# Kernel optimization log

Measured on AMD Instinct MI355X. Metric: run time of the kernel, lower is better.

## Reference

```python
import jax, jax.numpy as jnp
import numpy as np

NUM_HEADS = 4
HEAD_DIM = 64  # out_dim // num_heads
NEG_INF = -9e15


def setup_inputs() -> dict:
    key = jax.random.key(0)
    k1, k2, k3, k4 = jax.random.split(key, 4)
    b, n, in_dim, out_dim = 8, 1024, 256, 256
    x = jax.random.normal(k1, (b, n, in_dim), dtype=jnp.float32)
    adj = jax.random.uniform(k2, (b, n, n), dtype=jnp.float32)
    # linear_proj weight, stored as [in_dim, out_dim] (xavier-ish scale)
    Wp = jax.random.normal(k3, (in_dim, out_dim), dtype=jnp.float32) * (1.0 / np.sqrt(in_dim))
    # scoring_fn weight for concat([left(64), right(64), adj(1)]) -> 1
    Ws = jax.random.normal(k4, (2 * HEAD_DIM + 1,), dtype=jnp.float32) * (1.0 / np.sqrt(HEAD_DIM))
    bias = jnp.zeros((out_dim,), dtype=jnp.float32)
    return {"x": x, "adj": adj, "Wp": Wp, "Ws": Ws, "bias": bias}


def reference(x, adj, Wp, Ws, bias):
    b, n, _ = x.shape
    H, hd = NUM_HEADS, HEAD_DIM
    # manifold_in = Euclidean -> logmap0 is identity; dropout is eval (p=0)
    proj = (x @ Wp).reshape(b, n, H, hd)  # [b,n,H,hd]
    # scoring_fn(cat[left, right, adj]) decomposed: score = left.w_l + right.w_r + adj*w_a
    w_l, w_r, w_a = Ws[:hd], Ws[hd:2 * hd], Ws[2 * hd]
    s_l = jnp.einsum('bnhd,d->bnh', proj, w_l)  # dest-node term
    s_r = jnp.einsum('bmhd,d->bmh', proj, w_r)  # src-node term
    score = s_l[:, :, None, :] + s_r[:, None, :, :] + (adj * w_a)[..., None]  # [b,n,n,H]
    score = jax.nn.leaky_relu(score, 0.2)
    # local_agg: mask out non-edges (adj <= 1e-5) by adding -9e15
    pad = (adj <= 1e-5).astype(score.dtype)
    score = score + (NEG_INF * pad)[..., None]
    att = jax.nn.softmax(score, axis=2)  # softmax over source nodes m
    # msg[b,i,h,d] = sum_m att[b,i,m,h] * proj[b,m,h,d]
    msg = jnp.einsum('bimh,bmhd->bihd', att, proj).reshape(b, n, H * hd)
    # in_dim == out_dim -> no skip_proj; Euclidean expmap0/transp0/expmap: out = x + msg + bias
    out = x + msg + bias
    out = jax.nn.leaky_relu(out, 0.5)  # act = LeakyReLU(0.5)
    return out, adj
```

## Files before the change

kernel.cpp:

```cpp
#include <hip/hip_runtime.h>

#define NHEADS 4
#define HDIM   64
#define BATCH  8
#define SEQ    1024
#define CH     256
#define LOG2E  1.4426950408889634f
#define MC     128
#define LDP    132

typedef float  f32x4  __attribute__((ext_vector_type(4)));
typedef __bf16 bf16x8 __attribute__((ext_vector_type(8)));
typedef short  s16x8  __attribute__((ext_vector_type(8)));
union FU { s16x8 s; bf16x8 b; };

__device__ inline unsigned short f2bf(float f) {
    unsigned u = __float_as_uint(f);
    return (unsigned short)((u + 0x7fffu + ((u >> 16) & 1u)) >> 16);
}
__device__ inline float4 nt_load4(const float* p) {
    f32x4 v = __builtin_nontemporal_load(reinterpret_cast<const f32x4*>(p));
    return make_float4(v.x, v.y, v.z, v.w);
}
__device__ inline void nt_store4(float* p, float4 v) {
    f32x4 u = {v.x, v.y, v.z, v.w};
    __builtin_nontemporal_store(u, reinterpret_cast<f32x4*>(p));
}


__global__ __launch_bounds__(256) void wpt_cast(const float* __restrict__ Wp,
                                                unsigned short* __restrict__ WpT) {
    __shared__ float T[32][33];
    const int t = threadIdx.x;
    const int kt = blockIdx.x * 32, ct = blockIdx.y * 32;
    const int r = t >> 3, c4 = (t & 7) * 4;
    float4 v = *reinterpret_cast<const float4*>(&Wp[(size_t)(kt + r) * CH + ct + c4]);
    T[r][c4 + 0] = v.x; T[r][c4 + 1] = v.y; T[r][c4 + 2] = v.z; T[r][c4 + 3] = v.w;
    __syncthreads();
    unsigned p0 = (unsigned)f2bf(T[c4 + 0][r]) | ((unsigned)f2bf(T[c4 + 1][r]) << 16);
    unsigned p1 = (unsigned)f2bf(T[c4 + 2][r]) | ((unsigned)f2bf(T[c4 + 3][r]) << 16);
    uint2 o = make_uint2(p0, p1);
    *reinterpret_cast<uint2*>(&WpT[(size_t)(ct + r) * CH + kt + c4]) = o;
}

__global__ __launch_bounds__(256, 2) void proj_fused(const float* __restrict__ x,
                                                     const unsigned short* __restrict__ WpT,
                                                     const float* __restrict__ Ws,
                                                     unsigned short* __restrict__ projT,
                                                     float* __restrict__ sl,
                                                     float* __restrict__ sr) {
    const int t = threadIdx.x, w = t >> 6, l = t & 63, il = l & 15, g = l >> 4;
    const int row0 = blockIdx.x * 16;
    const int b = row0 >> 10, n0 = row0 & 1023;

    const unsigned short* Ap = WpT + (size_t)(w * 64 + il) * CH + g * 8;
    const float*          Bp = x + (size_t)(row0 + il) * CH + g * 8;

    float4 xv[8][2];
#pragma unroll
    for (int kt = 0; kt < 8; ++kt) {
        xv[kt][0] = *reinterpret_cast<const float4*>(Bp + kt * 32);
        xv[kt][1] = *reinterpret_cast<const float4*>(Bp + kt * 32 + 4);
    }

    f32x4 acc[4] = {};
#pragma unroll
    for (int kt = 0; kt < 8; ++kt) {
        FU a[4], bb;
#pragma unroll
        for (int ai = 0; ai < 4; ++ai)
            a[ai].s = *reinterpret_cast<const s16x8*>(Ap + (size_t)ai * 16 * CH + kt * 32);
        bb.b[0] = (__bf16)xv[kt][0].x; bb.b[1] = (__bf16)xv[kt][0].y;
        bb.b[2] = (__bf16)xv[kt][0].z; bb.b[3] = (__bf16)xv[kt][0].w;
        bb.b[4] = (__bf16)xv[kt][1].x; bb.b[5] = (__bf16)xv[kt][1].y;
        bb.b[6] = (__bf16)xv[kt][1].z; bb.b[7] = (__bf16)xv[kt][1].w;
#pragma unroll
        for (int ai = 0; ai < 4; ++ai)
            acc[ai] = __builtin_amdgcn_mfma_f32_16x16x32_bf16(a[ai].b, bb.b, acc[ai], 0, 0, 0);
    }

    unsigned short* pS = projT + (((size_t)(b * NHEADS + w)) << 16)
                       + (size_t)(n0 >> 4) * 1024 + (il >> 3) * 128 + (il & 7);
#pragma unroll
    for (int ai = 0; ai < 4; ++ai)
#pragma unroll
        for (int q = 0; q < 4; ++q)
            pS[ai * 256 + (g * 4 + q) * 8] = f2bf(acc[ai][q]);

    float pl = 0.f, pr = 0.f;
#pragma unroll
    for (int ai = 0; ai < 4; ++ai) {
        float4 wlv = *reinterpret_cast<const float4*>(&Ws[ai * 16 + g * 4]);
        float4 wrv = *reinterpret_cast<const float4*>(&Ws[HDIM + ai * 16 + g * 4]);
        pl += acc[ai][0] * wlv.x + acc[ai][1] * wlv.y + acc[ai][2] * wlv.z + acc[ai][3] * wlv.w;
        pr += acc[ai][0] * wrv.x + acc[ai][1] * wrv.y + acc[ai][2] * wrv.z + acc[ai][3] * wrv.w;
    }
    pl += __shfl_xor(pl, 16); pl += __shfl_xor(pl, 32);
    pr += __shfl_xor(pr, 16); pr += __shfl_xor(pr, 32);
    if (l < 16) {
        sl[(size_t)(b * NHEADS + w) * SEQ + n0 + il] = pl * LOG2E;
        sr[(size_t)(b * NHEADS + w) * SEQ + n0 + il] = pr * LOG2E;
    }
}

template <bool FUSE_ADJ>
__global__ __launch_bounds__(512, 2) void attn13(const float* __restrict__ x,
                                                 const float* __restrict__ adj,
                                                 const unsigned short* __restrict__ projT,
                                                 const float* __restrict__ sl,
                                                 const float* __restrict__ sr,
                                                 const float* __restrict__ Ws,
                                                 const float* __restrict__ bias,
                                                 float* __restrict__ out,
                                                 float* __restrict__ out_adj) {
    __shared__ __align__(16) float abuf[2][2][16][LDP];

    const int t = threadIdx.x;
    const int w = t >> 6, l = t & 63, il = l & 15, g = l >> 4;
    const int h = w & 3, mh = w >> 2;
    const int b  = blockIdx.x & 7;
    const int i0 = (blockIdx.x >> 3) * 16;
    const float wa2 = Ws[2 * HDIM] * LOG2E;

    const int sh = t >> 8;
    const int str = (t >> 4) & 15;
    const int stc = (t & 15) * 4;
    const size_t astg = ((size_t)(b * SEQ + i0 + str)) * SEQ + sh * 512 + stc;

    const float sl_i = sl[(size_t)(b * NHEADS + h) * SEQ + i0 + il];
    const float* srp = sr + (size_t)(b * NHEADS + h) * SEQ + mh * 512;
    const unsigned short* pTsw = projT + (((size_t)(b * NHEADS + h)) << 16)
                               + (size_t)mh * 32768
                               + (g >> 1) * 1024 + (g & 1) * 128 + il * 8;

    FU ones;
#pragma unroll
    for (int j = 0; j < 8; ++j) ones.s[j] = (short)0x3F80;

    f32x4 acc[4] = {};
    f32x4 dacc = {};

    float4 c00 = nt_load4(adj + astg);
    float4 c01 = nt_load4(adj + astg + 64);
    float4 cur0 = nt_load4(adj + astg + MC);
    float4 cur1 = nt_load4(adj + astg + MC + 64);
    if (FUSE_ADJ) {
        nt_store4(out_adj + astg, c00);
        nt_store4(out_adj + astg + 64, c01);
    }
    *reinterpret_cast<float4*>(&abuf[0][sh][str][stc])      = c00;
    *reinterpret_cast<float4*>(&abuf[0][sh][str][stc + 64]) = c01;
    __syncthreads();

    for (int c = 0; c < 4; ++c) {
        float4 nx0 = {}, nx1 = {};
        if (c + 2 < 4) {
            nx0 = nt_load4(adj + astg + (size_t)(c + 2) * MC);
            nx1 = nt_load4(adj + astg + (size_t)(c + 2) * MC + 64);
        }
        const float* aT = &abuf[c & 1][mh][il][0];
        const int mt = c * MC;

        float4 av[4][2], sv4[4][2];
        FU B[4][4];
#pragma unroll
        for (int kq = 0; kq < 4; ++kq) {
            const int mk = kq * 32 + g * 8;
            av[kq][0]  = *reinterpret_cast<const float4*>(aT + mk);
            av[kq][1]  = *reinterpret_cast<const float4*>(aT + mk + 4);
            sv4[kq][0] = *reinterpret_cast<const float4*>(srp + mt + mk);
            sv4[kq][1] = *reinterpret_cast<const float4*>(srp + mt + mk + 4);
        }
#pragma unroll
        for (int kq = 0; kq < 4; ++kq) {
#pragma unroll
            for (int bj = 0; bj < 4; ++bj)
                B[kq][bj].s = *reinterpret_cast<const s16x8*>(
                    pTsw + c * 8192 + kq * 2048 + bj * 256);
        }

        FU af[4];
#pragma unroll
        for (int kq = 0; kq < 4; ++kq) {
            float aj[8] = {av[kq][0].x, av[kq][0].y, av[kq][0].z, av[kq][0].w,
                           av[kq][1].x, av[kq][1].y, av[kq][1].z, av[kq][1].w};
            float sv[8] = {sv4[kq][0].x, sv4[kq][0].y, sv4[kq][0].z, sv4[kq][0].w,
                           sv4[kq][1].x, sv4[kq][1].y, sv4[kq][1].z, sv4[kq][1].w};
#pragma unroll
            for (int j = 0; j < 8; ++j) {
                float s = fmaf(aj[j], wa2, sl_i + sv[j]);
                s = __builtin_amdgcn_fmed3f(s, 0.2f * s, 86.5617f);
                float e = (aj[j] <= 1e-5f) ? 0.f : __builtin_amdgcn_exp2f(s);
                af[kq].b[j] = (__bf16)e;
            }
        }

#pragma unroll
        for (int kq = 0; kq < 4; ++kq) {
            acc[0] = __builtin_amdgcn_mfma_f32_16x16x32_bf16(af[kq].b, B[kq][0].b, acc[0], 0, 0, 0);
            acc[1] = __builtin_amdgcn_mfma_f32_16x16x32_bf16(af[kq].b, B[kq][1].b, acc[1], 0, 0, 0);
            acc[2] = __builtin_amdgcn_mfma_f32_16x16x32_bf16(af[kq].b, B[kq][2].b, acc[2], 0, 0, 0);
            acc[3] = __builtin_amdgcn_mfma_f32_16x16x32_bf16(af[kq].b, B[kq][3].b, acc[3], 0, 0, 0);
            dacc   = __builtin_amdgcn_mfma_f32_16x16x32_bf16(af[kq].b, ones.b,   dacc,   0, 0, 0);
        }

        if (c + 1 < 4) {
            if (FUSE_ADJ) {
                nt_store4(out_adj + astg + (size_t)(c + 1) * MC, cur0);
                nt_store4(out_adj + astg + (size_t)(c + 1) * MC + 64, cur1);
            }
            *reinterpret_cast<float4*>(&abuf[(c + 1) & 1][sh][str][stc])      = cur0;
            *reinterpret_cast<float4*>(&abuf[(c + 1) & 1][sh][str][stc + 64]) = cur1;
        }
        __syncthreads();
        cur0 = nx0; cur1 = nx1;
    }

    float (*part)[16][68] = reinterpret_cast<float (*)[16][68]>(&abuf[0][0][0][0]);
    if (mh == 1) {
#pragma unroll
        for (int bj = 0; bj < 4; ++bj)
#pragma unroll
            for (int q = 0; q < 4; ++q)
                part[h][g * 4 + q][bj * 16 + il] = acc[bj][q];
        if (il == 0) {
#pragma unroll
            for (int q = 0; q < 4; ++q) part[h][g * 4 + q][64] = dacc[q];
        }
    }
    __syncthreads();
    if (mh == 0) {
        const float* bb = bias + h * HDIM;
#pragma unroll
        for (int q = 0; q < 4; ++q) {
            const int row = g * 4 + q;
            const float den = dacc[q] + part[h][row][64];
            const float inv = 1.f / den;
            const size_t ob = ((size_t)(b * SEQ + i0 + row)) * CH + h * HDIM + il;
#pragma unroll
            for (int bj = 0; bj < 4; ++bj) {
                float m = acc[bj][q] + part[h][row][bj * 16 + il];
                float v = fmaf(m, inv, x[ob + bj * 16] + bb[bj * 16 + il]);
                v = fmaxf(v, 0.5f * v);
                __builtin_nontemporal_store(v, out + ob + bj * 16);
            }
        }
    }
}

__global__ void adjcopy(const float* __restrict__ adj, float* __restrict__ dst, int n4) {
    int idx = blockIdx.x * blockDim.x + threadIdx.x;
    int stride = gridDim.x * blockDim.x;
    const float4* s = reinterpret_cast<const float4*>(adj);
    float4* d = reinterpret_cast<float4*>(dst);
    for (int i = idx; i < n4; i += stride) d[i] = s[i];
}

extern "C" void kernel_launch(void* const* d_in, const int* in_sizes, int n_in,
                              void* d_out, int out_size, void* d_ws, size_t ws_size,
                              hipStream_t stream) {
    const float* x    = (const float*)d_in[0];
    const float* adj  = (const float*)d_in[1];
    const float* Wp   = (const float*)d_in[2];
    const float* Ws   = (const float*)d_in[3];
    const float* bias = (const float*)d_in[4];
    float* out     = (float*)d_out;
    float* out_adj = out + (size_t)BATCH * SEQ * CH;

    const size_t nProj = (size_t)BATCH * SEQ * CH;
    const size_t nSc   = (size_t)BATCH * NHEADS * SEQ;
    const size_t need  = CH * CH * 2 + nProj * 2 + 2 * nSc * 4;
    const bool use_ws  = (ws_size >= need);
    char* scratch = use_ws ? (char*)d_ws : (char*)out_adj;
    unsigned short* WpT   = (unsigned short*)scratch;
    unsigned short* projT = (unsigned short*)(scratch + (size_t)CH * CH * 2);
    float*          sl    = (float*)(scratch + (size_t)CH * CH * 2 + nProj * 2);
    float*          sr    = sl + nSc;

    wpt_cast<<<dim3(8, 8), 256, 0, stream>>>(Wp, WpT);
    proj_fused<<<dim3(512), 256, 0, stream>>>(x, WpT, Ws, projT, sl, sr);
    if (use_ws) {
        attn13<true><<<dim3(512), 512, 0, stream>>>(
            x, adj, projT, sl, sr, Ws, bias, out, out_adj);
    } else {
        attn13<false><<<dim3(512), 512, 0, stream>>>(
            x, adj, projT, sl, sr, Ws, bias, out, out_adj);
        adjcopy<<<2048, 256, 0, stream>>>(adj, out_adj, (BATCH * SEQ * SEQ) / 4);
    }
}
```

Before: 51.26 us.

## Move adj passthrough copy into projection kernel and use cached adj loads

```diff
diff --git a/kernel.cpp b/kernel.cpp
--- a/kernel.cpp
+++ b/kernel.cpp
@@ -17,10 +17,6 @@
 __device__ inline unsigned short f2bf(float f) {
     unsigned u = __float_as_uint(f);
     return (unsigned short)((u + 0x7fffu + ((u >> 16) & 1u)) >> 16);
-}
-__device__ inline float4 nt_load4(const float* p) {
-    f32x4 v = __builtin_nontemporal_load(reinterpret_cast<const f32x4*>(p));
-    return make_float4(v.x, v.y, v.z, v.w);
 }
 __device__ inline void nt_store4(float* p, float4 v) {
     f32x4 u = {v.x, v.y, v.z, v.w};
@@ -43,12 +39,15 @@
     *reinterpret_cast<uint2*>(&WpT[(size_t)(ct + r) * CH + kt + c4]) = o;
 }
 
+template <bool COPY>
 __global__ __launch_bounds__(256, 2) void proj_fused(const float* __restrict__ x,
                                                      const unsigned short* __restrict__ WpT,
                                                      const float* __restrict__ Ws,
+                                                     const float* __restrict__ adj,
                                                      unsigned short* __restrict__ projT,
                                                      float* __restrict__ sl,
-                                                     float* __restrict__ sr) {
+                                                     float* __restrict__ sr,
+                                                     float* __restrict__ out_adj) {
     const int t = threadIdx.x, w = t >> 6, l = t & 63, il = l & 15, g = l >> 4;
     const int row0 = blockIdx.x * 16;
     const int b = row0 >> 10, n0 = row0 & 1023;
@@ -101,18 +100,31 @@
         sl[(size_t)(b * NHEADS + w) * SEQ + n0 + il] = pl * LOG2E;
         sr[(size_t)(b * NHEADS + w) * SEQ + n0 + il] = pr * LOG2E;
     }
-}
-
-template <bool FUSE_ADJ>
-__global__ __launch_bounds__(512, 2) void attn13(const float* __restrict__ x,
+
+    if (COPY) {
+        const float4* csrc = reinterpret_cast<const float4*>(adj) + (size_t)blockIdx.x * 4096;
+        float*        cdst = out_adj + (size_t)blockIdx.x * 16384;
+#pragma unroll
+        for (int sweep = 0; sweep < 2; ++sweep) {
+            float4 C[8];
+#pragma unroll
+            for (int k = 0; k < 8; ++k)
+                C[k] = csrc[sweep * 2048 + k * 256 + t];
+#pragma unroll
+            for (int k = 0; k < 8; ++k)
+                nt_store4(cdst + (size_t)(sweep * 2048 + k * 256 + t) * 4, C[k]);
+        }
+    }
+}
+
+__global__ __launch_bounds__(512, 2) void attn15(const float* __restrict__ x,
                                                  const float* __restrict__ adj,
                                                  const unsigned short* __restrict__ projT,
                                                  const float* __restrict__ sl,
                                                  const float* __restrict__ sr,
                                                  const float* __restrict__ Ws,
                                                  const float* __restrict__ bias,
-                                                 float* __restrict__ out,
-                                                 float* __restrict__ out_adj) {
+                                                 float* __restrict__ out) {
     __shared__ __align__(16) float abuf[2][2][16][LDP];
 
     const int t = threadIdx.x;
@@ -140,14 +152,10 @@
     f32x4 acc[4] = {};
     f32x4 dacc = {};
 
-    float4 c00 = nt_load4(adj + astg);
-    float4 c01 = nt_load4(adj + astg + 64);
-    float4 cur0 = nt_load4(adj + astg + MC);
-    float4 cur1 = nt_load4(adj + astg + MC + 64);
-    if (FUSE_ADJ) {
-        nt_store4(out_adj + astg, c00);
-        nt_store4(out_adj + astg + 64, c01);
-    }
+    float4 c00 = *reinterpret_cast<const float4*>(adj + astg);
+    float4 c01 = *reinterpret_cast<const float4*>(adj + astg + 64);
+    float4 cur0 = *reinterpret_cast<const float4*>(adj + astg + MC);
+    float4 cur1 = *reinterpret_cast<const float4*>(adj + astg + MC + 64);
     *reinterpret_cast<float4*>(&abuf[0][sh][str][stc])      = c00;
     *reinterpret_cast<float4*>(&abuf[0][sh][str][stc + 64]) = c01;
     __syncthreads();
@@ -155,8 +163,8 @@
     for (int c = 0; c < 4; ++c) {
         float4 nx0 = {}, nx1 = {};
         if (c + 2 < 4) {
-            nx0 = nt_load4(adj + astg + (size_t)(c + 2) * MC);
-            nx1 = nt_load4(adj + astg + (size_t)(c + 2) * MC + 64);
+            nx0 = *reinterpret_cast<const float4*>(adj + astg + (size_t)(c + 2) * MC);
+            nx1 = *reinterpret_cast<const float4*>(adj + astg + (size_t)(c + 2) * MC + 64);
         }
         const float* aT = &abuf[c & 1][mh][il][0];
         const int mt = c * MC;
@@ -205,10 +213,6 @@
         }
 
         if (c + 1 < 4) {
-            if (FUSE_ADJ) {
-                nt_store4(out_adj + astg + (size_t)(c + 1) * MC, cur0);
-                nt_store4(out_adj + astg + (size_t)(c + 1) * MC + 64, cur1);
-            }
             *reinterpret_cast<float4*>(&abuf[(c + 1) & 1][sh][str][stc])      = cur0;
             *reinterpret_cast<float4*>(&abuf[(c + 1) & 1][sh][str][stc + 64]) = cur1;
         }
@@ -278,13 +282,16 @@
     float*          sr    = sl + nSc;
 
     wpt_cast<<<dim3(8, 8), 256, 0, stream>>>(Wp, WpT);
-    proj_fused<<<dim3(512), 256, 0, stream>>>(x, WpT, Ws, projT, sl, sr);
     if (use_ws) {
-        attn13<true><<<dim3(512), 512, 0, stream>>>(
-            x, adj, projT, sl, sr, Ws, bias, out, out_adj);
+        proj_fused<true><<<dim3(512), 256, 0, stream>>>(
+            x, WpT, Ws, adj, projT, sl, sr, out_adj);
+        attn15<<<dim3(512), 512, 0, stream>>>(
+            x, adj, projT, sl, sr, Ws, bias, out);
     } else {
-        attn13<false><<<dim3(512), 512, 0, stream>>>(
-            x, adj, projT, sl, sr, Ws, bias, out, out_adj);
+        proj_fused<false><<<dim3(512), 256, 0, stream>>>(
+            x, WpT, Ws, adj, projT, sl, sr, out_adj);
+        attn15<<<dim3(512), 512, 0, stream>>>(
+            x, adj, projT, sl, sr, Ws, bias, out);
         adjcopy<<<2048, 256, 0, stream>>>(adj, out_adj, (BATCH * SEQ * SEQ) / 4);
     }
 }
```

Result: no change. 52.08 us (+1.6%).
